# Kernel optimization log

Measured on AMD Instinct MI355X. Metric: run time of the kernel, lower is better.

## Reference

```python
import jax, jax.numpy as jnp
import numpy as np

B, N, D = 16, 2048, 64

def setup_inputs() -> dict:
    key = jax.random.key(0)
    kq, kk, kv = jax.random.split(key, 3)
    queries = jax.random.normal(kq, (B, N, D), dtype=jnp.float32)
    keys = jax.random.normal(kk, (B, N, D), dtype=jnp.float32)
    values = jax.random.normal(kv, (B, N, D), dtype=jnp.float32)
    scaling_factor = jnp.asarray(np.sqrt(D), dtype=jnp.float32)
    return {"queries": queries, "keys": keys, "values": values, "scaling_factor": scaling_factor}

def reference(queries, keys, values, scaling_factor):
    # scores: [B, N, N] = Q K^T / scale
    scores = jnp.einsum('bqd,bkd->bqk', queries, keys) / scaling_factor
    atn = jax.nn.softmax(scores, axis=2)
    return jnp.einsum('bqk,bkd->bqd', atn, values)
```

## Files before the change

### kernel.cpp

```cpp
#include <hip/hip_runtime.h>
#include <hip/hip_bf16.h>

#define BATCH 16
#define SEQ 2048
#define DIM 64

typedef __attribute__((ext_vector_type(8))) __bf16 bf16x8;
typedef __attribute__((ext_vector_type(8))) unsigned short u16x8;
typedef __attribute__((ext_vector_type(4))) unsigned int u32x4;
typedef __attribute__((ext_vector_type(16))) float f32x16;

#if __has_builtin(__builtin_amdgcn_exp2f)
#define EXP2F(x) __builtin_amdgcn_exp2f(x)
#else
#define EXP2F(x) __expf(0.69314718055994531f * (x))
#endif

__device__ __forceinline__ unsigned short f2bf_hw(float f) {
    __bf16 h = (__bf16)f;
    return __builtin_bit_cast(unsigned short, h);
}

__device__ __forceinline__ unsigned int pk_bf16(float lo, float hi) {
    unsigned int a = f2bf_hw(lo), b = f2bf_hw(hi);
    return a | (b << 16);
}

__device__ __forceinline__ bf16x8 ld_bf8_g(const unsigned short* p) {
    u16x8 u = *(const u16x8*)p;
    return __builtin_bit_cast(bf16x8, u);
}

__global__ __launch_bounds__(256)
void preconvert_kv(const float* __restrict__ K, const float* __restrict__ V,
                   unsigned short* __restrict__ Ks, unsigned short* __restrict__ Vts) {
    __shared__ float vt[128 * 65];
    const int tid = threadIdx.x;
    const int b = blockIdx.x >> 4;
    const int t = blockIdx.x & 15;
    const int kt = t * 128;

    {
        const float* src = V + ((size_t)(b * SEQ + kt)) * DIM;
        #pragma unroll
        for (int p = 0; p < 8; ++p) {
            const int f = p * 256 + tid;
            const int row = f >> 4, c4 = (f & 15) << 2;
            float4 x = *(const float4*)(src + row * DIM + c4);
            vt[row * 65 + c4 + 0] = x.x; vt[row * 65 + c4 + 1] = x.y;
            vt[row * 65 + c4 + 2] = x.z; vt[row * 65 + c4 + 3] = x.w;
        }
    }
    {
        const float* src = K + ((size_t)(b * SEQ + kt)) * DIM;
        unsigned short* dst = Ks + ((size_t)(b * 16 + t)) * 8192;
        #pragma unroll
        for (int p = 0; p < 4; ++p) {
            const int cid = p * 256 + tid;
            const int key = cid >> 3, g = cid & 7;
            const int d0 = (g >> 1) * 16 + (g & 1) * 8;
            float4 x0 = *(const float4*)(src + key * DIM + d0);
            float4 x1 = *(const float4*)(src + key * DIM + d0 + 4);
            u16x8 o;
            o[0] = f2bf_hw(x0.x); o[1] = f2bf_hw(x0.y); o[2] = f2bf_hw(x0.z); o[3] = f2bf_hw(x0.w);
            o[4] = f2bf_hw(x1.x); o[5] = f2bf_hw(x1.y); o[6] = f2bf_hw(x1.z); o[7] = f2bf_hw(x1.w);
            *(u16x8*)(dst + (g * 128 + key) * 8) = o;
        }
    }
    __syncthreads();
    {
        unsigned short* dst = Vts + ((size_t)(b * 16 + t)) * 8192;
        #pragma unroll
        for (int p = 0; p < 4; ++p) {
            const int cid = p * 256 + tid;
            const int g = cid >> 6, d = cid & 63;
            const int k0 = (g >> 1) * 16 + (g & 1) * 8;
            u16x8 o;
            #pragma unroll
            for (int j = 0; j < 8; ++j) o[j] = f2bf_hw(vt[(k0 + j) * 65 + d]);
            *(u16x8*)(dst + (g * 64 + d) * 8) = o;
        }
    }
}

__global__ __launch_bounds__(256, 2)
void attn_flash_kernel(const float* __restrict__ Q,
                       const unsigned short* __restrict__ Ks,
                       const unsigned short* __restrict__ Vts,
                       const float* __restrict__ scaling,
                       float* __restrict__ O) {
    __shared__ float comb[3 * 64 * 66];

    const int tid  = threadIdx.x;
    const int w    = tid >> 6;
    const int lane = tid & 63;
    const int m    = lane & 31;
    const int h    = lane >> 5;

    const int x  = blockIdx.x;
    const int b  = ((x & 7) << 1) | ((x >> 3) & 1);
    const int q0 = (x >> 4) * 64;

    const float csc = 1.4426950408889634f / scaling[0];

    bf16x8 aq0[4], aq1[4];
    #pragma unroll
    for (int s = 0; s < 2; ++s) {
        const float* qsrc = Q + ((size_t)(b * SEQ + q0 + s * 32 + m)) * DIM + h * 8;
        #pragma unroll
        for (int c = 0; c < 4; ++c) {
            float4 x0 = *(const float4*)(qsrc + c * 16);
            float4 x1 = *(const float4*)(qsrc + c * 16 + 4);
            u32x4 pk;
            pk[0] = pk_bf16(x0.x * csc, x0.y * csc);
            pk[1] = pk_bf16(x0.z * csc, x0.w * csc);
            pk[2] = pk_bf16(x1.x * csc, x1.y * csc);
            pk[3] = pk_bf16(x1.z * csc, x1.w * csc);
            (s ? aq1 : aq0)[c] = __builtin_bit_cast(bf16x8, pk);
        }
    }

    f32x16 Oacc0[2], Oacc1[2];
    #pragma unroll
    for (int dt = 0; dt < 2; ++dt)
        #pragma unroll
        for (int r = 0; r < 16; ++r) { Oacc0[dt][r] = 0.f; Oacc1[dt][r] = 0.f; }
    float psum0 = 0.f, psum1 = 0.f;

    const unsigned short* Kbase = Ks + ((size_t)(b * 16 + w * 4)) * 8192;
    const unsigned short* Vbase = Vts + ((size_t)(b * 16 + w * 4)) * 8192;

    for (int it = 0; it < 4; ++it) {
        const unsigned short* Kt = Kbase + (size_t)it * 8192;
        const unsigned short* Vt = Vbase + (size_t)it * 8192;
        #pragma unroll
        for (int t = 0; t < 4; ++t) {
            f32x16 S0, S1;
            #pragma unroll
            for (int r = 0; r < 16; ++r) { S0[r] = 0.f; S1[r] = 0.f; }
            #pragma unroll
            for (int c = 0; c < 4; ++c) {
                bf16x8 bk = ld_bf8_g(&Kt[((c * 2 + h) * 128 + t * 32 + m) * 8]);
                S0 = __builtin_amdgcn_mfma_f32_32x32x16_bf16(bk, aq0[c], S0, 0, 0, 0);
                S1 = __builtin_amdgcn_mfma_f32_32x32x16_bf16(bk, aq1[c], S1, 0, 0, 0);
            }
            unsigned int d0a[8], d0b[8], dsa[8], dsb[8];
            #pragma unroll
            for (int k = 0; k < 4; ++k) {
                float a0 = EXP2F(S0[4 * k + 0]), a1 = EXP2F(S0[4 * k + 1]);
                float a2 = EXP2F(S0[4 * k + 2]), a3 = EXP2F(S0[4 * k + 3]);
                psum0 += (a0 + a1) + (a2 + a3);
                d0a[2 * k + 0] = pk_bf16(a0, a1);
                d0a[2 * k + 1] = pk_bf16(a2, a3);
                float b0 = EXP2F(S1[4 * k + 0]), b1 = EXP2F(S1[4 * k + 1]);
                float b2 = EXP2F(S1[4 * k + 2]), b3 = EXP2F(S1[4 * k + 3]);
                psum1 += (b0 + b1) + (b2 + b3);
                d0b[2 * k + 0] = pk_bf16(b0, b1);
                d0b[2 * k + 1] = pk_bf16(b2, b3);
            }
            #pragma unroll
            for (int i = 0; i < 8; ++i) {
                dsa[i] = (unsigned int)__shfl_xor((int)d0a[i], 32);
                dsb[i] = (unsigned int)__shfl_xor((int)d0b[i], 32);
            }
            #pragma unroll
            for (int c2 = 0; c2 < 2; ++c2) {
                u32x4 bw0, bw1;
                bw0[0] = h ? dsa[4 * c2 + 2] : d0a[4 * c2 + 0];
                bw0[1] = h ? dsa[4 * c2 + 3] : d0a[4 * c2 + 1];
                bw0[2] = h ? d0a[4 * c2 + 2] : dsa[4 * c2 + 0];
                bw0[3] = h ? d0a[4 * c2 + 3] : dsa[4 * c2 + 1];
                bw1[0] = h ? dsb[4 * c2 + 2] : d0b[4 * c2 + 0];
                bw1[1] = h ? dsb[4 * c2 + 3] : d0b[4 * c2 + 1];
                bw1[2] = h ? d0b[4 * c2 + 2] : dsb[4 * c2 + 0];
                bw1[3] = h ? d0b[4 * c2 + 3] : dsb[4 * c2 + 1];
                bf16x8 pb0 = __builtin_bit_cast(bf16x8, bw0);
                bf16x8 pb1 = __builtin_bit_cast(bf16x8, bw1);
                const int kc = 2 * t + c2;
                #pragma unroll
                for (int dt = 0; dt < 2; ++dt) {
                    bf16x8 bv = ld_bf8_g(&Vt[((kc * 2 + h) * 64 + dt * 32 + m) * 8]);
                    Oacc0[dt] = __builtin_amdgcn_mfma_f32_32x32x16_bf16(bv, pb0, Oacc0[dt], 0, 0, 0);
                    Oacc1[dt] = __builtin_amdgcn_mfma_f32_32x32x16_bf16(bv, pb1, Oacc1[dt], 0, 0, 0);
                }
            }
        }
    }

    float l0 = psum0 + __shfl_xor(psum0, 32);
    float l1 = psum1 + __shfl_xor(psum1, 32);
    if (w > 0) {
        float* dst = comb + ((w - 1) * 64 + lane) * 66;
        #pragma unroll
        for (int dt = 0; dt < 2; ++dt)
            #pragma unroll
            for (int r = 0; r < 16; ++r) {
                dst[dt * 16 + r]      = Oacc0[dt][r];
                dst[33 + dt * 16 + r] = Oacc1[dt][r];
            }
        dst[32] = l0;
        dst[65] = l1;
    }
    __syncthreads();
    if (w == 0) {
        const float* p0 = comb + (0 * 64 + lane) * 66;
        const float* p1 = comb + (1 * 64 + lane) * 66;
        const float* p2 = comb + (2 * 64 + lane) * 66;
        const float invl0 = 1.0f / (l0 + p0[32] + p1[32] + p2[32]);
        const float invl1 = 1.0f / (l1 + p0[65] + p1[65] + p2[65]);
        float* orow0 = O + ((size_t)(b * SEQ + q0 + m)) * DIM;
        float* orow1 = O + ((size_t)(b * SEQ + q0 + 32 + m)) * DIM;
        #pragma unroll
        for (int dt = 0; dt < 2; ++dt) {
            #pragma unroll
            for (int k = 0; k < 4; ++k) {
                float4 o4;
                #pragma unroll
                for (int j = 0; j < 4; ++j) {
                    const int r = 4 * k + j;
                    ((float*)&o4)[j] = (Oacc0[dt][r] + p0[dt * 16 + r] + p1[dt * 16 + r]
                                        + p2[dt * 16 + r]) * invl0;
                }
                *(float4*)(orow0 + dt * 32 + 8 * k + 4 * h) = o4;
                #pragma unroll
                for (int j = 0; j < 4; ++j) {
                    const int r = 4 * k + j;
                    ((float*)&o4)[j] = (Oacc1[dt][r] + p0[33 + dt * 16 + r] + p1[33 + dt * 16 + r]
                                        + p2[33 + dt * 16 + r]) * invl1;
                }
                *(float4*)(orow1 + dt * 32 + 8 * k + 4 * h) = o4;
            }
        }
    }
}

extern "C" void kernel_launch(void* const* d_in, const int* in_sizes, int n_in,
                              void* d_out, int out_size, void* d_ws, size_t ws_size,
                              hipStream_t stream) {
    const float* Q = (const float*)d_in[0];
    const float* K = (const float*)d_in[1];
    const float* V = (const float*)d_in[2];
    const float* scaling = (const float*)d_in[3];
    float* O = (float*)d_out;

    unsigned short* Ks  = (unsigned short*)d_ws;
    unsigned short* Vts = Ks + (size_t)BATCH * 16 * 8192;

    preconvert_kv<<<dim3(BATCH * 16), dim3(256), 0, stream>>>(K, V, Ks, Vts);
    attn_flash_kernel<<<dim3(BATCH * (SEQ / 64)), dim3(256), 0, stream>>>(Q, Ks, Vts, scaling, O);
}
```

Measured before the change: 107.5 us.

## Prefetch next K tile in registers and split K/V preconversion across blocks

The attention inner loop is flattened into a 16-step non-unrolled loop. Each step prefetches the next K tile's bf16 fragments into registers and issues the V loads before the exp/softmax work, so global load latency overlaps with computation. The preconvert kernel now uses 512 blocks, one set for K and one for V, which doubles parallelism, and the K blocks no longer wait on a barrier. Costs are higher register pressure from the prefetched fragments, which could hurt occupancy at 2 blocks per CU, and possible loss of unrolling benefits.

```diff
diff --git a/kernel.cpp b/kernel.cpp
--- a/kernel.cpp
+++ b/kernel.cpp
@@ -36,23 +36,10 @@
                    unsigned short* __restrict__ Ks, unsigned short* __restrict__ Vts) {
     __shared__ float vt[128 * 65];
     const int tid = threadIdx.x;
-    const int b = blockIdx.x >> 4;
-    const int t = blockIdx.x & 15;
-    const int kt = t * 128;
-
-    {
-        const float* src = V + ((size_t)(b * SEQ + kt)) * DIM;
-        #pragma unroll
-        for (int p = 0; p < 8; ++p) {
-            const int f = p * 256 + tid;
-            const int row = f >> 4, c4 = (f & 15) << 2;
-            float4 x = *(const float4*)(src + row * DIM + c4);
-            vt[row * 65 + c4 + 0] = x.x; vt[row * 65 + c4 + 1] = x.y;
-            vt[row * 65 + c4 + 2] = x.z; vt[row * 65 + c4 + 3] = x.w;
-        }
-    }
-    {
-        const float* src = K + ((size_t)(b * SEQ + kt)) * DIM;
+    if (blockIdx.x < 256) {
+        const int b = blockIdx.x >> 4;
+        const int t = blockIdx.x & 15;
+        const float* src = K + ((size_t)(b * SEQ + t * 128)) * DIM;
         unsigned short* dst = Ks + ((size_t)(b * 16 + t)) * 8192;
         #pragma unroll
         for (int p = 0; p < 4; ++p) {
@@ -66,9 +53,20 @@
             o[4] = f2bf_hw(x1.x); o[5] = f2bf_hw(x1.y); o[6] = f2bf_hw(x1.z); o[7] = f2bf_hw(x1.w);
             *(u16x8*)(dst + (g * 128 + key) * 8) = o;
         }
-    }
-    __syncthreads();
-    {
+    } else {
+        const int vb = blockIdx.x - 256;
+        const int b = vb >> 4;
+        const int t = vb & 15;
+        const float* src = V + ((size_t)(b * SEQ + t * 128)) * DIM;
+        #pragma unroll
+        for (int p = 0; p < 8; ++p) {
+            const int f = p * 256 + tid;
+            const int row = f >> 4, c4 = (f & 15) << 2;
+            float4 x = *(const float4*)(src + row * DIM + c4);
+            vt[row * 65 + c4 + 0] = x.x; vt[row * 65 + c4 + 1] = x.y;
+            vt[row * 65 + c4 + 2] = x.z; vt[row * 65 + c4 + 3] = x.w;
+        }
+        __syncthreads();
         unsigned short* dst = Vts + ((size_t)(b * 16 + t)) * 8192;
         #pragma unroll
         for (int p = 0; p < 4; ++p) {
@@ -130,61 +128,81 @@
     const unsigned short* Kbase = Ks + ((size_t)(b * 16 + w * 4)) * 8192;
     const unsigned short* Vbase = Vts + ((size_t)(b * 16 + w * 4)) * 8192;
 
-    for (int it = 0; it < 4; ++it) {
-        const unsigned short* Kt = Kbase + (size_t)it * 8192;
+    bf16x8 kc[4];
+    #pragma unroll
+    for (int c = 0; c < 4; ++c)
+        kc[c] = ld_bf8_g(&Kbase[((c * 2 + h) * 128 + m) * 8]);
+
+    #pragma unroll 1
+    for (int st = 0; st < 16; ++st) {
+        const int it = st >> 2, t = st & 3;
         const unsigned short* Vt = Vbase + (size_t)it * 8192;
-        #pragma unroll
-        for (int t = 0; t < 4; ++t) {
-            f32x16 S0, S1;
-            #pragma unroll
-            for (int r = 0; r < 16; ++r) { S0[r] = 0.f; S1[r] = 0.f; }
-            #pragma unroll
-            for (int c = 0; c < 4; ++c) {
-                bf16x8 bk = ld_bf8_g(&Kt[((c * 2 + h) * 128 + t * 32 + m) * 8]);
-                S0 = __builtin_amdgcn_mfma_f32_32x32x16_bf16(bk, aq0[c], S0, 0, 0, 0);
-                S1 = __builtin_amdgcn_mfma_f32_32x32x16_bf16(bk, aq1[c], S1, 0, 0, 0);
+
+        f32x16 S0, S1;
+        #pragma unroll
+        for (int r = 0; r < 16; ++r) { S0[r] = 0.f; S1[r] = 0.f; }
+        #pragma unroll
+        for (int c = 0; c < 4; ++c) {
+            S0 = __builtin_amdgcn_mfma_f32_32x32x16_bf16(kc[c], aq0[c], S0, 0, 0, 0);
+            S1 = __builtin_amdgcn_mfma_f32_32x32x16_bf16(kc[c], aq1[c], S1, 0, 0, 0);
+        }
+
+        const int stn = (st < 15) ? st + 1 : 15;
+        const unsigned short* Ktn = Kbase + (size_t)(stn >> 2) * 8192;
+        const int tn = stn & 3;
+        bf16x8 kn[4];
+        #pragma unroll
+        for (int c = 0; c < 4; ++c)
+            kn[c] = ld_bf8_g(&Ktn[((c * 2 + h) * 128 + tn * 32 + m) * 8]);
+
+        bf16x8 bv[2][2];
+        #pragma unroll
+        for (int c2 = 0; c2 < 2; ++c2)
+            #pragma unroll
+            for (int dt = 0; dt < 2; ++dt)
+                bv[c2][dt] = ld_bf8_g(&Vt[(((2 * t + c2) * 2 + h) * 64 + dt * 32 + m) * 8]);
+
+        unsigned int d0a[8], d0b[8], dsa[8], dsb[8];
+        #pragma unroll
+        for (int k = 0; k < 4; ++k) {
+            float a0 = EXP2F(S0[4 * k + 0]), a1 = EXP2F(S0[4 * k + 1]);
+            float a2 = EXP2F(S0[4 * k + 2]), a3 = EXP2F(S0[4 * k + 3]);
+            psum0 += (a0 + a1) + (a2 + a3);
+            d0a[2 * k + 0] = pk_bf16(a0, a1);
+            d0a[2 * k + 1] = pk_bf16(a2, a3);
+            float b0 = EXP2F(S1[4 * k + 0]), b1 = EXP2F(S1[4 * k + 1]);
+            float b2 = EXP2F(S1[4 * k + 2]), b3 = EXP2F(S1[4 * k + 3]);
+            psum1 += (b0 + b1) + (b2 + b3);
+            d0b[2 * k + 0] = pk_bf16(b0, b1);
+            d0b[2 * k + 1] = pk_bf16(b2, b3);
+        }
+        #pragma unroll
+        for (int i = 0; i < 8; ++i) {
+            dsa[i] = (unsigned int)__shfl_xor((int)d0a[i], 32);
+            dsb[i] = (unsigned int)__shfl_xor((int)d0b[i], 32);
+        }
+        #pragma unroll
+        for (int c2 = 0; c2 < 2; ++c2) {
+            u32x4 bw0, bw1;
+            bw0[0] = h ? dsa[4 * c2 + 2] : d0a[4 * c2 + 0];
+            bw0[1] = h ? dsa[4 * c2 + 3] : d0a[4 * c2 + 1];
+            bw0[2] = h ? d0a[4 * c2 + 2] : dsa[4 * c2 + 0];
+            bw0[3] = h ? d0a[4 * c2 + 3] : dsa[4 * c2 + 1];
+            bw1[0] = h ? dsb[4 * c2 + 2] : d0b[4 * c2 + 0];
+            bw1[1] = h ? dsb[4 * c2 + 3] : d0b[4 * c2 + 1];
+            bw1[2] = h ? d0b[4 * c2 + 2] : dsb[4 * c2 + 0];
+            bw1[3] = h ? d0b[4 * c2 + 3] : dsb[4 * c2 + 1];
+            bf16x8 pb0 = __builtin_bit_cast(bf16x8, bw0);
+            bf16x8 pb1 = __builtin_bit_cast(bf16x8, bw1);
+            #pragma unroll
+            for (int dt = 0; dt < 2; ++dt) {
+                Oacc0[dt] = __builtin_amdgcn_mfma_f32_32x32x16_bf16(bv[c2][dt], pb0, Oacc0[dt], 0, 0, 0);
+                Oacc1[dt] = __builtin_amdgcn_mfma_f32_32x32x16_bf16(bv[c2][dt], pb1, Oacc1[dt], 0, 0, 0);
             }
-            unsigned int d0a[8], d0b[8], dsa[8], dsb[8];
-            #pragma unroll
-            for (int k = 0; k < 4; ++k) {
-                float a0 = EXP2F(S0[4 * k + 0]), a1 = EXP2F(S0[4 * k + 1]);
-                float a2 = EXP2F(S0[4 * k + 2]), a3 = EXP2F(S0[4 * k + 3]);
-                psum0 += (a0 + a1) + (a2 + a3);
-                d0a[2 * k + 0] = pk_bf16(a0, a1);
-                d0a[2 * k + 1] = pk_bf16(a2, a3);
-                float b0 = EXP2F(S1[4 * k + 0]), b1 = EXP2F(S1[4 * k + 1]);
-                float b2 = EXP2F(S1[4 * k + 2]), b3 = EXP2F(S1[4 * k + 3]);
-                psum1 += (b0 + b1) + (b2 + b3);
-                d0b[2 * k + 0] = pk_bf16(b0, b1);
-                d0b[2 * k + 1] = pk_bf16(b2, b3);
-            }
-            #pragma unroll
-            for (int i = 0; i < 8; ++i) {
-                dsa[i] = (unsigned int)__shfl_xor((int)d0a[i], 32);
-                dsb[i] = (unsigned int)__shfl_xor((int)d0b[i], 32);
-            }
-            #pragma unroll
-            for (int c2 = 0; c2 < 2; ++c2) {
-                u32x4 bw0, bw1;
-                bw0[0] = h ? dsa[4 * c2 + 2] : d0a[4 * c2 + 0];
-                bw0[1] = h ? dsa[4 * c2 + 3] : d0a[4 * c2 + 1];
-                bw0[2] = h ? d0a[4 * c2 + 2] : dsa[4 * c2 + 0];
-                bw0[3] = h ? d0a[4 * c2 + 3] : dsa[4 * c2 + 1];
-                bw1[0] = h ? dsb[4 * c2 + 2] : d0b[4 * c2 + 0];
-                bw1[1] = h ? dsb[4 * c2 + 3] : d0b[4 * c2 + 1];
-                bw1[2] = h ? d0b[4 * c2 + 2] : dsb[4 * c2 + 0];
-                bw1[3] = h ? d0b[4 * c2 + 3] : dsb[4 * c2 + 1];
-                bf16x8 pb0 = __builtin_bit_cast(bf16x8, bw0);
-                bf16x8 pb1 = __builtin_bit_cast(bf16x8, bw1);
-                const int kc = 2 * t + c2;
-                #pragma unroll
-                for (int dt = 0; dt < 2; ++dt) {
-                    bf16x8 bv = ld_bf8_g(&Vt[((kc * 2 + h) * 64 + dt * 32 + m) * 8]);
-                    Oacc0[dt] = __builtin_amdgcn_mfma_f32_32x32x16_bf16(bv, pb0, Oacc0[dt], 0, 0, 0);
-                    Oacc1[dt] = __builtin_amdgcn_mfma_f32_32x32x16_bf16(bv, pb1, Oacc1[dt], 0, 0, 0);
-                }
-            }
-        }
+        }
+
+        #pragma unroll
+        for (int c = 0; c < 4; ++c) kc[c] = kn[c];
     }
 
     float l0 = psum0 + __shfl_xor(psum0, 32);
@@ -246,6 +264,6 @@
     unsigned short* Ks  = (unsigned short*)d_ws;
     unsigned short* Vts = Ks + (size_t)BATCH * 16 * 8192;
 
-    preconvert_kv<<<dim3(BATCH * 16), dim3(256), 0, stream>>>(K, V, Ks, Vts);
+    preconvert_kv<<<dim3(512), dim3(256), 0, stream>>>(K, V, Ks, Vts);
     attn_flash_kernel<<<dim3(BATCH * (SEQ / 64)), dim3(256), 0, stream>>>(Q, Ks, Vts, scaling, O);
 }
```

After: 104.3 us. 3.0% less time.
